# Kernel tuning notes

Hardware: AMD Instinct MI355X
Metric: run time of the kernel (lower is better)

The kernel has to match this reference:

```python
import jax, jax.numpy as jnp
import numpy as np
import math

B, S, D, H = 4, 2048, 1024, 16
HD = D // H  # 64
MOD_DIMS = [("text", 768, 2048), ("image", 1024, 1024), ("audio", 512, 1500), ("video", 2048, 512)]
M = len(MOD_DIMS)
WIN, DEPTH = 3, 8


def _cantor_routes():
    coords = []
    for i in range(M):
        x = i / max(1, M - 1)
        x = max(1e-06, min(x, 1.0 - 1e-06))
        val, f = 0.0, 0.5
        for _ in range(DEPTH):
            x *= 3.0
            d = int(x)
            x -= d
            if d == 2:
                val += f
            f *= 0.5
        coords.append(val)
    c = np.asarray(coords, dtype=np.float32)
    dist = np.abs(c[:, None] - c[None, :])
    # topk smallest distances (stable tie-break like torch ascending sort)
    return np.argsort(dist, axis=1, kind="stable")[:, :WIN]

ROUTES = jnp.asarray(_cantor_routes())


def setup_inputs() -> dict:
    key = jax.random.key(0)
    ks = iter(jax.random.split(key, 32))
    inp = {}
    for name, dim, sl in MOD_DIMS:
        inp[name] = jax.random.normal(next(ks), (B, sl, dim), dtype=jnp.float32)
        inp[f"W_{name}"] = jax.random.normal(next(ks), (D, dim), dtype=jnp.float32) / math.sqrt(dim)
        inp[f"b_{name}"] = jnp.zeros((D,), dtype=jnp.float32)
    inp["mod_emb"] = jax.random.normal(next(ks), (M, D), dtype=jnp.float32) * 0.02
    for nm in ("q", "k", "v", "o"):
        inp[f"W{nm}"] = jax.random.normal(next(ks), (D, D), dtype=jnp.float32) / math.sqrt(D)
        inp[f"b{nm}"] = jnp.zeros((D,), dtype=jnp.float32)
    inp["temperature"] = jnp.asarray(0.07, dtype=jnp.float32)
    return inp


def reference(text, image, audio, video, W_text, b_text, W_image, b_image,
              W_audio, b_audio, W_video, b_video, mod_emb, Wq, bq, Wk, bk,
              Wv, bv, Wo, bo, temperature):
    xs = [text, image, audio, video]
    Ws = [W_text, W_image, W_audio, W_video]
    bs = [b_text, b_image, b_audio, b_video]
    projected = []
    for i in range(M):
        p = xs[i] @ Ws[i].T + bs[i] + mod_emb[i]          # [B, s_i, D]
        p = jnp.pad(p, ((0, 0), (0, S - p.shape[1]), (0, 0)))
        projected.append(p)
    stacked = jnp.stack(projected, axis=1)                # [B, M, S, D]

    def heads(x, W, b):
        return (x @ W.T + b).reshape(B, M, S, H, HD).transpose(0, 3, 1, 2, 4)  # [B,H,M,S,HD]

    Q = heads(stacked, Wq, bq)
    K = heads(stacked, Wk, bk)
    V = heads(stacked, Wv, bv)

    Kn = K[:, :, ROUTES]
    Vn = V[:, :, ROUTES]
    scores = jnp.einsum('bhmsd,bhmwsd->bhmsw', Q, Kn) / (math.sqrt(HD) * jnp.abs(temperature))
    attn = jax.nn.softmax(scores, axis=-1)                # dropout is identity at eval
    out = jnp.einsum('bhmsw,bhmwsd->bhmsd', attn, Vn)     # [B,H,M,S,HD]
    fused = out.mean(axis=2)                              # [B,H,S,HD]
    fused = fused.transpose(0, 2, 1, 3).reshape(B, S, D)
    return fused @ Wo.T + bo
```

## Files before the change

kernel.cpp:

```cpp
#include <hip/hip_runtime.h>

typedef unsigned short u16;
typedef __bf16 bf16x8 __attribute__((ext_vector_type(8)));
typedef u16   u16x8  __attribute__((ext_vector_type(8)));
typedef u16   u16x4  __attribute__((ext_vector_type(4)));
typedef float f32x4  __attribute__((ext_vector_type(4)));

#define RPB 5084
#define SL0 2048
#define SL1 1024
#define SL2 1500
#define SL3 512

__device__ __forceinline__ u16 f2bf(float f) {
  union { float f; unsigned u; } x; x.f = f;
  unsigned u = x.u;
  u += 0x7fffu + ((u >> 16) & 1u);
  return (u16)(u >> 16);
}
__device__ __forceinline__ float bf2f(u16 h) {
  union { unsigned u; float f; } x; x.u = ((unsigned)h) << 16;
  return x.f;
}
__device__ __forceinline__ void gll16(const u16* g, u16* l) {
  __builtin_amdgcn_global_load_lds(
      (const __attribute__((address_space(1))) void*)g,
      (__attribute__((address_space(3))) void*)l, 16, 0, 0);
}


#define NSEG 12
struct CvtSegs {
  const float* src[NSEG];
  u16*         dst[NSEG];
  int          blk_end[NSEG];
  int          blk_base[NSEG];
};
__global__ __launch_bounds__(256) void cvt_multi(CvtSegs segs) {
  int blk = blockIdx.x, seg = 0;
#pragma unroll
  for (int s = 0; s < NSEG; ++s) if (blk >= segs.blk_end[s]) seg = s + 1;
  const float* src = segs.src[seg];
  u16* dst = segs.dst[seg];
  int i = (blk - segs.blk_base[seg]) * 1024 + threadIdx.x * 4;
  f32x4 v = *(const f32x4*)(src + i);
  u16x4 o;
  o[0] = f2bf(v[0]); o[1] = f2bf(v[1]); o[2] = f2bf(v[2]); o[3] = f2bf(v[3]);
  *(u16x4*)(dst + i) = o;
}

template<int STORE_F32>
__global__ __launch_bounds__(256) void gemm_lds(
    const u16* __restrict__ A,
    const u16* __restrict__ B0, const u16* __restrict__ B1, const u16* __restrict__ B2,
    const float* __restrict__ c0, const float* __restrict__ c1, const float* __restrict__ c2,
    void* __restrict__ Cout, int Mr, int K, int ldc)
{
  __shared__ u16 lA0[128 * 32], lA1[128 * 32];
  __shared__ u16 lB0[128 * 32], lB1[128 * 32];
  const int tid  = threadIdx.x;
  const int lane = tid & 63;
  const int wave = tid >> 6;
  const int wr   = (wave >> 1) * 64;
  const int wc   = (wave & 1) * 64;
  const int row0 = blockIdx.y * 128;

  const int wsel = blockIdx.x >> 3;
  const int colL = (blockIdx.x & 7) * 128;
  const u16*   Bw   = (wsel == 0) ? B0 : (wsel == 1) ? B1 : B2;
  const float* bias = (wsel == 0) ? c0 : (wsel == 1) ? c1 : c2;

  const int srow = lane >> 2;
  const int soct = (((lane & 3) ^ ((lane >> 3) & 3))) << 3;
  int ra0 = row0 + wave * 32 + srow;      if (ra0 >= Mr) ra0 = Mr - 1;
  int ra1 = row0 + wave * 32 + srow + 16; if (ra1 >= Mr) ra1 = Mr - 1;
  const u16* pA0 = A + (size_t)ra0 * K + soct;
  const u16* pA1 = A + (size_t)ra1 * K + soct;
  const u16* pB0 = Bw + (size_t)(colL + wave * 32 + srow) * K + soct;
  const u16* pB1 = pB0 + (size_t)16 * K;
  u16* dA0a = &lA0[(wave * 32) * 32];      u16* dA1a = &lA0[(wave * 32 + 16) * 32];
  u16* dA0b = &lA1[(wave * 32) * 32];      u16* dA1b = &lA1[(wave * 32 + 16) * 32];
  u16* dB0a = &lB0[(wave * 32) * 32];      u16* dB1a = &lB0[(wave * 32 + 16) * 32];
  u16* dB0b = &lB1[(wave * 32) * 32];      u16* dB1b = &lB1[(wave * 32 + 16) * 32];

  f32x4 acc[4][4];
#pragma unroll
  for (int i = 0; i < 4; ++i)
#pragma unroll
    for (int j = 0; j < 4; ++j) acc[i][j] = f32x4{0.f, 0.f, 0.f, 0.f};

  const int fr  = lane & 15;
  const int fo  = lane >> 4;
  const int lrd = fr * 32 + (((fo ^ ((fr >> 1) & 3))) << 3);
  const int ca  = (wr >> 4) * 512;
  const int cbb = (wc >> 4) * 512;

  for (int k0 = 0; k0 < K; k0 += 64) {
    __syncthreads();
    gll16(pA0 + k0, dA0a);       gll16(pA1 + k0, dA1a);
    gll16(pB0 + k0, dB0a);       gll16(pB1 + k0, dB1a);
    gll16(pA0 + k0 + 32, dA0b);  gll16(pA1 + k0 + 32, dA1b);
    gll16(pB0 + k0 + 32, dB0b);  gll16(pB1 + k0 + 32, dB1b);
    __syncthreads();

    bf16x8 af[4], bfr[4];
#pragma unroll
    for (int j = 0; j < 4; ++j)
      bfr[j] = *(const bf16x8*)&lB0[cbb + j * 512 + lrd];
#pragma unroll
    for (int i = 0; i < 4; ++i)
      af[i] = *(const bf16x8*)&lA0[ca + i * 512 + lrd];
#pragma unroll
    for (int i = 0; i < 4; ++i)
#pragma unroll
      for (int j = 0; j < 4; ++j)
        acc[i][j] = __builtin_amdgcn_mfma_f32_16x16x32_bf16(af[i], bfr[j], acc[i][j], 0, 0, 0);
#pragma unroll
    for (int j = 0; j < 4; ++j)
      bfr[j] = *(const bf16x8*)&lB1[cbb + j * 512 + lrd];
#pragma unroll
    for (int i = 0; i < 4; ++i)
      af[i] = *(const bf16x8*)&lA1[ca + i * 512 + lrd];
#pragma unroll
    for (int i = 0; i < 4; ++i)
#pragma unroll
      for (int j = 0; j < 4; ++j)
        acc[i][j] = __builtin_amdgcn_mfma_f32_16x16x32_bf16(af[i], bfr[j], acc[i][j], 0, 0, 0);
  }

  const int fc = lane & 15;
  const int rq = (lane >> 4) * 4;
#pragma unroll
  for (int i = 0; i < 4; ++i) {
#pragma unroll
    for (int j = 0; j < 4; ++j) {
      const int cl = wc + j * 16 + fc;
      const float badd = bias[colL + cl];
      const int gc = blockIdx.x * 128 + cl;
#pragma unroll
      for (int reg = 0; reg < 4; ++reg) {
        int gr = row0 + wr + i * 16 + rq + reg;
        if (gr < Mr) {
          float v = acc[i][j][reg] + badd;
          if (STORE_F32) ((float*)Cout)[(size_t)gr * ldc + gc] = v;
          else           ((u16*)Cout)[(size_t)gr * ldc + gc] = f2bf(v);
        }
      }
    }
  }
}

__global__ __launch_bounds__(512, 2) void gemm_qkv_256(
    const u16* __restrict__ A,
    const u16* __restrict__ B0, const u16* __restrict__ B1, const u16* __restrict__ B2,
    const float* __restrict__ c0, const float* __restrict__ c1, const float* __restrict__ c2,
    u16* __restrict__ C, int Mr, int K)
{
  __shared__ u16 lds[4][2][8192];
  const int tid  = threadIdx.x;
  const int lane = tid & 63;
  const int wave = tid >> 6;
  const int wm   = wave >> 2;
  const int wn   = wave & 3;
  const int row0 = blockIdx.y * 256;
  const int cb   = blockIdx.x;
  const int wsel = cb >> 2;
  const int colL = (cb & 3) * 256;
  const u16*   Bw   = (wsel == 0) ? B0 : (wsel == 1) ? B1 : B2;
  const float* bias = (wsel == 0) ? c0 : (wsel == 1) ? c1 : c2;

  const int srow = lane >> 2;
  const int soct = (((lane & 3) ^ ((lane >> 3) & 3))) << 3;
  int ra0 = row0 + wave * 16 + srow;        if (ra0 >= Mr) ra0 = Mr - 1;
  int ra1 = row0 + 128 + wave * 16 + srow;  if (ra1 >= Mr) ra1 = Mr - 1;
  const u16* pA0 = A + (size_t)ra0 * K + soct;
  const u16* pA1 = A + (size_t)ra1 * K + soct;
  const u16* pB0 = Bw + (size_t)(colL + wave * 16 + srow) * K + soct;
  const u16* pB1 = pB0 + (size_t)128 * K;
  const int NS = K >> 5;

#define QSTAGE(slot, k0) do {                                   \
    gll16(pA0 + (k0), (u16*)&lds[slot][0][wave * 512]);         \
    gll16(pA1 + (k0), (u16*)&lds[slot][0][4096 + wave * 512]);  \
    gll16(pB0 + (k0), (u16*)&lds[slot][1][wave * 512]);         \
    gll16(pB1 + (k0), (u16*)&lds[slot][1][4096 + wave * 512]);  \
  } while (0)

  f32x4 acc[8][4];
#pragma unroll
  for (int m = 0; m < 8; ++m)
#pragma unroll
    for (int n = 0; n < 4; ++n) acc[m][n] = f32x4{0.f, 0.f, 0.f, 0.f};

  QSTAGE(0, 0);
  QSTAGE(1, 32);
  QSTAGE(2, 64);

  const int fr  = lane & 15;
  const int fo  = lane >> 4;
  const int lrd = fr * 32 + (((fo ^ ((fr >> 1) & 3))) << 3);
  const int cam = wm * 8 * 512;
  const int cbn = wn * 4 * 512;

#pragma unroll 4
  for (int s = 0; s < NS; ++s) {
    asm volatile("s_waitcnt vmcnt(8)" ::: "memory");
    __builtin_amdgcn_s_barrier();
    asm volatile("" ::: "memory");

    const u16* Ab = &lds[s & 3][0][0];
    const u16* Bb = &lds[s & 3][1][0];
    bf16x8 af[8], bf[4];
#pragma unroll
    for (int n = 0; n < 4; ++n)
      bf[n] = *(const bf16x8*)&Bb[cbn + n * 512 + lrd];
#pragma unroll
    for (int m = 0; m < 8; ++m)
      af[m] = *(const bf16x8*)&Ab[cam + m * 512 + lrd];

    const int s3 = s + 3;
    const int k3 = (s3 < NS ? s3 : NS - 1) << 5;
    QSTAGE(s3 & 3, k3);

#pragma unroll
    for (int m = 0; m < 8; ++m)
#pragma unroll
      for (int n = 0; n < 4; ++n)
        acc[m][n] = __builtin_amdgcn_mfma_f32_16x16x32_bf16(af[m], bf[n], acc[m][n], 0, 0, 0);
  }
#undef QSTAGE

  asm volatile("s_waitcnt vmcnt(0)" ::: "memory");

  const int fc = lane & 15;
  const int rq = (lane >> 4) * 4;
#pragma unroll
  for (int m = 0; m < 8; ++m) {
#pragma unroll
    for (int n = 0; n < 4; ++n) {
      const int cl = wn * 64 + n * 16 + fc;
      const float badd = bias[colL + cl];
      const int gc = cb * 256 + cl;
#pragma unroll
      for (int reg = 0; reg < 4; ++reg) {
        int gr = row0 + wm * 128 + m * 16 + rq + reg;
        if (gr < Mr)
          C[(size_t)gr * 3072 + gc] = f2bf(acc[m][n][reg] + badd);
      }
    }
  }
}

struct ProjSegs {
  const u16*   A[4];
  const u16*   Bw[4];
  const float* b0[4];
  const float* b1[4];
  int Mr[4], K[4], sl[4], obase[4];
  int blk_end[4];
};
__global__ __launch_bounds__(256) void gemm_proj_all(ProjSegs ps, u16* __restrict__ Cout) {
  int blk = blockIdx.x, seg = 0;
#pragma unroll
  for (int s = 0; s < 3; ++s) if (blk >= ps.blk_end[s]) seg = s + 1;
  const int base  = seg ? ps.blk_end[seg - 1] : 0;
  const int local = blk - base;
  const int row0  = (local >> 3) * 128;
  const int col0  = (local & 7) * 128;
  const int Mr = ps.Mr[seg], K = ps.K[seg], sl = ps.sl[seg], obase = ps.obase[seg];
  const u16* A  = ps.A[seg];
  const u16* Bw = ps.Bw[seg];
  const float* bias0 = ps.b0[seg];
  const float* bias1 = ps.b1[seg];

  __shared__ u16 lA0[128 * 32], lA1[128 * 32];
  __shared__ u16 lB0[128 * 32], lB1[128 * 32];
  const int tid  = threadIdx.x;
  const int lane = tid & 63;
  const int wave = tid >> 6;
  const int wr   = (wave >> 1) * 64;
  const int wc   = (wave & 1) * 64;

  const int srow = lane >> 2;
  const int soct = (((lane & 3) ^ ((lane >> 3) & 3))) << 3;
  int ra0 = row0 + wave * 32 + srow;      if (ra0 >= Mr) ra0 = Mr - 1;
  int ra1 = row0 + wave * 32 + srow + 16; if (ra1 >= Mr) ra1 = Mr - 1;
  const u16* pA0 = A + (size_t)ra0 * K + soct;
  const u16* pA1 = A + (size_t)ra1 * K + soct;
  const u16* pB0 = Bw + (size_t)(col0 + wave * 32 + srow) * K + soct;
  const u16* pB1 = pB0 + (size_t)16 * K;
  u16* dA0a = &lA0[(wave * 32) * 32];      u16* dA1a = &lA0[(wave * 32 + 16) * 32];
  u16* dA0b = &lA1[(wave * 32) * 32];      u16* dA1b = &lA1[(wave * 32 + 16) * 32];
  u16* dB0a = &lB0[(wave * 32) * 32];      u16* dB1a = &lB0[(wave * 32 + 16) * 32];
  u16* dB0b = &lB1[(wave * 32) * 32];      u16* dB1b = &lB1[(wave * 32 + 16) * 32];

  f32x4 acc[4][4];
#pragma unroll
  for (int i = 0; i < 4; ++i)
#pragma unroll
    for (int j = 0; j < 4; ++j) acc[i][j] = f32x4{0.f, 0.f, 0.f, 0.f};

  const int fr  = lane & 15;
  const int fo  = lane >> 4;
  const int lrd = fr * 32 + (((fo ^ ((fr >> 1) & 3))) << 3);
  const int ca  = (wr >> 4) * 512;
  const int cbb = (wc >> 4) * 512;

  for (int k0 = 0; k0 < K; k0 += 64) {
    __syncthreads();
    gll16(pA0 + k0, dA0a);       gll16(pA1 + k0, dA1a);
    gll16(pB0 + k0, dB0a);       gll16(pB1 + k0, dB1a);
    gll16(pA0 + k0 + 32, dA0b);  gll16(pA1 + k0 + 32, dA1b);
    gll16(pB0 + k0 + 32, dB0b);  gll16(pB1 + k0 + 32, dB1b);
    __syncthreads();

    bf16x8 af[4], bfr[4];
#pragma unroll
    for (int j = 0; j < 4; ++j)
      bfr[j] = *(const bf16x8*)&lB0[cbb + j * 512 + lrd];
#pragma unroll
    for (int i = 0; i < 4; ++i)
      af[i] = *(const bf16x8*)&lA0[ca + i * 512 + lrd];
#pragma unroll
    for (int i = 0; i < 4; ++i)
#pragma unroll
      for (int j = 0; j < 4; ++j)
        acc[i][j] = __builtin_amdgcn_mfma_f32_16x16x32_bf16(af[i], bfr[j], acc[i][j], 0, 0, 0);
#pragma unroll
    for (int j = 0; j < 4; ++j)
      bfr[j] = *(const bf16x8*)&lB1[cbb + j * 512 + lrd];
#pragma unroll
    for (int i = 0; i < 4; ++i)
      af[i] = *(const bf16x8*)&lA1[ca + i * 512 + lrd];
#pragma unroll
    for (int i = 0; i < 4; ++i)
#pragma unroll
      for (int j = 0; j < 4; ++j)
        acc[i][j] = __builtin_amdgcn_mfma_f32_16x16x32_bf16(af[i], bfr[j], acc[i][j], 0, 0, 0);
  }

  const int fc = lane & 15;
  const int rq = (lane >> 4) * 4;
#pragma unroll
  for (int i = 0; i < 4; ++i) {
#pragma unroll
    for (int j = 0; j < 4; ++j) {
      const int c = col0 + wc + j * 16 + fc;
      const float badd = bias0[c] + bias1[c];
#pragma unroll
      for (int reg = 0; reg < 4; ++reg) {
        int gr = row0 + wr + i * 16 + rq + reg;
        if (gr < Mr) {
          int bb = gr / sl, ss = gr - bb * sl;
          Cout[(size_t)(bb * RPB + obase + ss) * 1024 + c] = f2bf(acc[i][j][reg] + badd);
        }
      }
    }
  }
}

__global__ __launch_bounds__(256) void attn_fuse(
    const u16* __restrict__ QKV,
    u16* __restrict__ fused,
    const float* __restrict__ bq, const float* __restrict__ bk, const float* __restrict__ bv,
    const float* __restrict__ temp_ptr)
{
  const int ROUTE[4][3] = {{0,1,2},{0,1,2},{2,3,0},{3,2,0}};
  const int SLm[4]  = {SL0, SL1, SL2, SL3};
  const int OFFS[4] = {0, 2048, 3072, 4572};
  const int tid  = threadIdx.x;
  const int lane = tid & 63;
  const int wave = tid >> 6;
  const int bs   = blockIdx.x * 2 + (wave >> 1);
  const int s    = bs & 2047;
  const int b    = bs >> 11;
  const int h    = (wave & 1) * 8 + (lane >> 3);
  const int sub  = lane & 7;
  const int dbase = h * 64 + sub * 8;
  const float scale = 1.0f / (8.0f * fabsf(temp_ptr[0]));

  float qf[4][8], kf[4][8], vf[4][8];
#pragma unroll
  for (int r = 0; r < 4; ++r) {
    if (s < SLm[r]) {
      const u16* base = QKV + ((size_t)(b * RPB + OFFS[r] + s)) * 3072 + dbase;
      u16x8 q8 = *(const u16x8*)(base);
      u16x8 k8 = *(const u16x8*)(base + 1024);
      u16x8 v8 = *(const u16x8*)(base + 2048);
#pragma unroll
      for (int i = 0; i < 8; ++i) {
        qf[r][i] = bf2f(q8[i]); kf[r][i] = bf2f(k8[i]); vf[r][i] = bf2f(v8[i]);
      }
    } else {
#pragma unroll
      for (int i = 0; i < 8; ++i) {
        qf[r][i] = bq[dbase + i]; kf[r][i] = bk[dbase + i]; vf[r][i] = bv[dbase + i];
      }
    }
  }

  float acc[8];
#pragma unroll
  for (int i = 0; i < 8; ++i) acc[i] = 0.f;

#pragma unroll
  for (int m = 0; m < 4; ++m) {
    float sc[3];
#pragma unroll
    for (int w = 0; w < 3; ++w) {
      const int r = ROUTE[m][w];
      float d = 0.f;
#pragma unroll
      for (int i = 0; i < 8; ++i) d += qf[m][i] * kf[r][i];
      d += __shfl_xor(d, 1, 64);
      d += __shfl_xor(d, 2, 64);
      d += __shfl_xor(d, 4, 64);
      sc[w] = d * scale;
    }
    float mx = fmaxf(sc[0], fmaxf(sc[1], sc[2]));
    float e0 = __expf(sc[0] - mx), e1 = __expf(sc[1] - mx), e2 = __expf(sc[2] - mx);
    float inv = 1.0f / (e0 + e1 + e2);
    float ws[3] = {e0 * inv, e1 * inv, e2 * inv};
#pragma unroll
    for (int w = 0; w < 3; ++w) {
      const int r = ROUTE[m][w];
#pragma unroll
      for (int i = 0; i < 8; ++i) acc[i] += ws[w] * vf[r][i];
    }
  }
  u16x8 o;
#pragma unroll
  for (int i = 0; i < 8; ++i) o[i] = f2bf(acc[i] * 0.25f);
  *(u16x8*)(fused + (size_t)bs * 1024 + dbase) = o;
}

extern "C" void kernel_launch(void* const* d_in, const int* in_sizes, int n_in,
                              void* d_out, int out_size, void* d_ws, size_t ws_size,
                              hipStream_t stream) {
  const int B = 4, S = 2048, D = 1024;
  const int SL[4]   = {SL0, SL1, SL2, SL3};
  const int DIM[4]  = {768, 1024, 512, 2048};
  const int OFFS[4] = {0, 2048, 3072, 4572};

  const float* x[4]  = {(const float*)d_in[0], (const float*)d_in[3], (const float*)d_in[6], (const float*)d_in[9]};
  const float* Wm[4] = {(const float*)d_in[1], (const float*)d_in[4], (const float*)d_in[7], (const float*)d_in[10]};
  const float* bm[4] = {(const float*)d_in[2], (const float*)d_in[5], (const float*)d_in[8], (const float*)d_in[11]};
  const float* mod_emb = (const float*)d_in[12];
  const float* Wq = (const float*)d_in[13]; const float* bq = (const float*)d_in[14];
  const float* Wk = (const float*)d_in[15]; const float* bk = (const float*)d_in[16];
  const float* Wv = (const float*)d_in[17]; const float* bv = (const float*)d_in[18];
  const float* Wo = (const float*)d_in[19]; const float* bo = (const float*)d_in[20];
  const float* temp = (const float*)d_in[21];

  const int RROWS = B * RPB;
  const size_t stackedB = ((size_t)RROWS * D * 2 + 255) / 256 * 256;
  const size_t qkvB     = ((size_t)RROWS * 3 * D * 2 + 255) / 256 * 256;
  const size_t wB       = ((size_t)D * D * 2 + 255) / 256 * 256;
  size_t wmB[4];
  for (int m = 0; m < 4; ++m) wmB[m] = ((size_t)D * DIM[m] * 2 + 255) / 256 * 256;
  const size_t need = stackedB + qkvB + 4 * wB + wmB[0] + wmB[1] + wmB[2] + wmB[3];
  if (ws_size < need) return;

  char* p = (char*)d_ws;
  u16* stacked = (u16*)p;  p += stackedB;
  char* qkvbase = p;
  u16* qkv     = (u16*)p;  p += qkvB;
  u16* wqb     = (u16*)p;  p += wB;
  u16* wkb     = (u16*)p;  p += wB;
  u16* wvb     = (u16*)p;  p += wB;
  u16* wob     = (u16*)p;  p += wB;
  u16* wmb[4];
  for (int m = 0; m < 4; ++m) { wmb[m] = (u16*)p; p += wmB[m]; }
  u16* fusedb  = stacked;

  u16* xb[4];
  {
    char* q = qkvbase;
    for (int m = 0; m < 4; ++m) {
      xb[m] = (u16*)q;
      q += ((size_t)B * SL[m] * DIM[m] * 2 + 255) / 256 * 256;
    }
  }

  {
    CvtSegs cs;
    const float* srcs[NSEG] = {x[0], x[1], x[2], x[3], Wm[0], Wm[1], Wm[2], Wm[3], Wq, Wk, Wv, Wo};
    u16* dsts[NSEG] = {xb[0], xb[1], xb[2], xb[3], wmb[0], wmb[1], wmb[2], wmb[3], wqb, wkb, wvb, wob};
    int ns[NSEG];
    for (int m = 0; m < 4; ++m) ns[m] = B * SL[m] * DIM[m];
    for (int m = 0; m < 4; ++m) ns[4 + m] = D * DIM[m];
    for (int i = 0; i < 4; ++i) ns[8 + i] = D * D;
    int base = 0;
    for (int i = 0; i < NSEG; ++i) {
      cs.src[i] = srcs[i]; cs.dst[i] = dsts[i];
      cs.blk_base[i] = base;
      base += (ns[i] + 1023) / 1024;
      cs.blk_end[i] = base;
    }
    cvt_multi<<<base, 256, 0, stream>>>(cs);
  }

  {
    const int ord[4] = {3, 1, 0, 2};
    ProjSegs ps;
    int base = 0;
    for (int i = 0; i < 4; ++i) {
      int m = ord[i];
      int Mr = B * SL[m];
      ps.A[i] = xb[m]; ps.Bw[i] = wmb[m];
      ps.b0[i] = bm[m]; ps.b1[i] = mod_emb + m * D;
      ps.Mr[i] = Mr; ps.K[i] = DIM[m]; ps.sl[i] = SL[m]; ps.obase[i] = OFFS[m];
      base += 8 * ((Mr + 127) / 128);
      ps.blk_end[i] = base;
    }
    gemm_proj_all<<<base, 256, 0, stream>>>(ps, stacked);
  }

  {
    dim3 grid(12, (RROWS + 255) / 256);
    gemm_qkv_256<<<grid, 512, 0, stream>>>(stacked, wqb, wkb, wvb, bq, bk, bv,
                                           qkv, RROWS, D);
  }

  attn_fuse<<<(B * S) / 2, 256, 0, stream>>>(qkv, fusedb, bq, bk, bv, temp);

  {
    dim3 grid(8, (B * S) / 128);
    gemm_lds<1><<<grid, 256, 0, stream>>>(fusedb, wob, wob, wob, bo, bo, bo,
                                          d_out, B * S, D, D);
  }
}
```

Before: 470.4 us.

## Restructure QKV GEMM into 8-phase ping-pong pipeline with XCD-aware block remap

```diff
diff --git a/kernel.cpp b/kernel.cpp
--- a/kernel.cpp
+++ b/kernel.cpp
@@ -150,20 +150,22 @@
   }
 }
 
-__global__ __launch_bounds__(512, 2) void gemm_qkv_256(
+__global__ __launch_bounds__(512, 2) void gemm_qkv_8ph(
     const u16* __restrict__ A,
     const u16* __restrict__ B0, const u16* __restrict__ B1, const u16* __restrict__ B2,
     const float* __restrict__ c0, const float* __restrict__ c1, const float* __restrict__ c2,
     u16* __restrict__ C, int Mr, int K)
 {
-  __shared__ u16 lds[4][2][8192];
+  __shared__ u16 lds[2][2][2][16][512];
   const int tid  = threadIdx.x;
   const int lane = tid & 63;
   const int wave = tid >> 6;
   const int wm   = wave >> 2;
   const int wn   = wave & 3;
-  const int row0 = blockIdx.y * 256;
-  const int cb   = blockIdx.x;
+
+  const int v    = (blockIdx.x & 7) * 120 + (blockIdx.x >> 3);
+  const int cb   = v % 12;
+  const int row0 = (v / 12) * 256;
   const int wsel = cb >> 2;
   const int colL = (cb & 3) * 256;
   const u16*   Bw   = (wsel == 0) ? B0 : (wsel == 1) ? B1 : B2;
@@ -177,58 +179,177 @@
   const u16* pA1 = A + (size_t)ra1 * K + soct;
   const u16* pB0 = Bw + (size_t)(colL + wave * 16 + srow) * K + soct;
   const u16* pB1 = pB0 + (size_t)128 * K;
-  const int NS = K >> 5;
-
-#define QSTAGE(slot, k0) do {                                   \
-    gll16(pA0 + (k0), (u16*)&lds[slot][0][wave * 512]);         \
-    gll16(pA1 + (k0), (u16*)&lds[slot][0][4096 + wave * 512]);  \
-    gll16(pB0 + (k0), (u16*)&lds[slot][1][wave * 512]);         \
-    gll16(pB1 + (k0), (u16*)&lds[slot][1][4096 + wave * 512]);  \
-  } while (0)
-
-  f32x4 acc[8][4];
-#pragma unroll
-  for (int m = 0; m < 8; ++m)
-#pragma unroll
-    for (int n = 0; n < 4; ++n) acc[m][n] = f32x4{0.f, 0.f, 0.f, 0.f};
-
-  QSTAGE(0, 0);
-  QSTAGE(1, 32);
-  QSTAGE(2, 64);
+
+#define STA(S, H, KK, KS) gll16(((H) ? pA1 : pA0) + (KK) + (KS) * 32, \
+                                (u16*)&lds[S][0][KS][(H) * 8 + wave][0])
+#define STB(S, H, KK, KS) gll16(((H) ? pB1 : pB0) + (KK) + (KS) * 32, \
+                                (u16*)&lds[S][1][KS][(H) * 8 + wave][0])
 
   const int fr  = lane & 15;
   const int fo  = lane >> 4;
   const int lrd = fr * 32 + (((fo ^ ((fr >> 1) & 3))) << 3);
-  const int cam = wm * 8 * 512;
-  const int cbn = wn * 4 * 512;
-
-#pragma unroll 4
-  for (int s = 0; s < NS; ++s) {
-    asm volatile("s_waitcnt vmcnt(8)" ::: "memory");
-    __builtin_amdgcn_s_barrier();
-    asm volatile("" ::: "memory");
-
-    const u16* Ab = &lds[s & 3][0][0];
-    const u16* Bb = &lds[s & 3][1][0];
-    bf16x8 af[8], bf[4];
-#pragma unroll
-    for (int n = 0; n < 4; ++n)
-      bf[n] = *(const bf16x8*)&Bb[cbn + n * 512 + lrd];
-#pragma unroll
-    for (int m = 0; m < 8; ++m)
-      af[m] = *(const bf16x8*)&Ab[cam + m * 512 + lrd];
-
-    const int s3 = s + 3;
-    const int k3 = (s3 < NS ? s3 : NS - 1) << 5;
-    QSTAGE(s3 & 3, k3);
-
-#pragma unroll
-    for (int m = 0; m < 8; ++m)
-#pragma unroll
-      for (int n = 0; n < 4; ++n)
-        acc[m][n] = __builtin_amdgcn_mfma_f32_16x16x32_bf16(af[m], bf[n], acc[m][n], 0, 0, 0);
-  }
-#undef QSTAGE
+  const int wm8 = wm * 8;
+  const int wn4 = wn * 4;
+
+#define LDA(S, M, KS) (*(const bf16x8*)&lds[S][0][KS][wm8 + (M)][lrd])
+#define LDB(S, N, KS) (*(const bf16x8*)&lds[S][1][KS][wn4 + (N)][lrd])
+
+  f32x4 acc[8][4];
+#pragma unroll
+  for (int m = 0; m < 8; ++m)
+#pragma unroll
+    for (int n = 0; n < 4; ++n) acc[m][n] = f32x4{0.f, 0.f, 0.f, 0.f};
+
+  STA(0, 0, 0, 0);  STA(0, 0, 0, 1);  STA(0, 1, 0, 0);  STA(0, 1, 0, 1);
+  STB(0, 0, 0, 0);  STB(0, 0, 0, 1);  STB(0, 1, 0, 0);  STB(0, 1, 0, 1);
+  STA(1, 0, 64, 0); STA(1, 0, 64, 1); STA(1, 1, 64, 0); STA(1, 1, 64, 1);
+  STB(1, 0, 64, 0); STB(1, 0, 64, 1); STB(1, 1, 64, 0); STB(1, 1, 64, 1);
+  asm volatile("s_waitcnt vmcnt(0)" ::: "memory");
+  __builtin_amdgcn_s_barrier();
+
+  bf16x8 af[4][2], bf[4][2];
+  const int NIT = K >> 7;
+
+#pragma unroll 1
+  for (int i = 0; i < NIT; ++i) {
+    const int k0  = i * 128;
+    const int kc2 = (k0 + 128 <= K - 64) ? k0 + 128 : K - 64;
+    const int kc3 = (k0 + 192 <= K - 64) ? k0 + 192 : K - 64;
+
+#pragma unroll
+    for (int m = 0; m < 4; ++m) { af[m][0] = LDA(0, m, 0); af[m][1] = LDA(0, m, 1); }
+#pragma unroll
+    for (int n = 0; n < 2; ++n) { bf[n][0] = LDB(0, n, 0); bf[n][1] = LDB(0, n, 1); }
+    if (i) { STA(1, 1, k0 + 64, 0); STA(1, 1, k0 + 64, 1); }
+    asm volatile("s_waitcnt lgkmcnt(8)" ::: "memory");
+    __builtin_amdgcn_s_barrier();
+    asm volatile("s_waitcnt lgkmcnt(0)" ::: "memory");
+    __builtin_amdgcn_s_setprio(1);
+#pragma unroll
+    for (int m = 0; m < 4; ++m)
+#pragma unroll
+      for (int n = 0; n < 2; ++n) {
+        acc[m][n] = __builtin_amdgcn_mfma_f32_16x16x32_bf16(af[m][0], bf[n][0], acc[m][n], 0, 0, 0);
+        acc[m][n] = __builtin_amdgcn_mfma_f32_16x16x32_bf16(af[m][1], bf[n][1], acc[m][n], 0, 0, 0);
+      }
+    __builtin_amdgcn_s_setprio(0);
+    __builtin_amdgcn_s_barrier();
+
+#pragma unroll
+    for (int n = 2; n < 4; ++n) { bf[n][0] = LDB(0, n, 0); bf[n][1] = LDB(0, n, 1); }
+    __builtin_amdgcn_s_barrier();
+    asm volatile("s_waitcnt lgkmcnt(0)" ::: "memory");
+    __builtin_amdgcn_s_setprio(1);
+#pragma unroll
+    for (int m = 0; m < 4; ++m)
+#pragma unroll
+      for (int n = 2; n < 4; ++n) {
+        acc[m][n] = __builtin_amdgcn_mfma_f32_16x16x32_bf16(af[m][0], bf[n][0], acc[m][n], 0, 0, 0);
+        acc[m][n] = __builtin_amdgcn_mfma_f32_16x16x32_bf16(af[m][1], bf[n][1], acc[m][n], 0, 0, 0);
+      }
+    __builtin_amdgcn_s_setprio(0);
+    __builtin_amdgcn_s_barrier();
+
+#pragma unroll
+    for (int m = 0; m < 4; ++m) { af[m][0] = LDA(0, 4 + m, 0); af[m][1] = LDA(0, 4 + m, 1); }
+    STB(0, 0, kc2, 0); STB(0, 0, kc2, 1);
+    __builtin_amdgcn_s_barrier();
+    asm volatile("s_waitcnt lgkmcnt(0)" ::: "memory");
+    __builtin_amdgcn_s_setprio(1);
+#pragma unroll
+    for (int m = 0; m < 4; ++m)
+#pragma unroll
+      for (int n = 0; n < 2; ++n) {
+        acc[4 + m][n] = __builtin_amdgcn_mfma_f32_16x16x32_bf16(af[m][0], bf[n][0], acc[4 + m][n], 0, 0, 0);
+        acc[4 + m][n] = __builtin_amdgcn_mfma_f32_16x16x32_bf16(af[m][1], bf[n][1], acc[4 + m][n], 0, 0, 0);
+      }
+    __builtin_amdgcn_s_setprio(0);
+    __builtin_amdgcn_s_barrier();
+
+    STB(0, 1, kc2, 0); STB(0, 1, kc2, 1);
+    STA(0, 0, kc2, 0); STA(0, 0, kc2, 1);
+    asm volatile("s_waitcnt vmcnt(6)" ::: "memory");
+    __builtin_amdgcn_s_barrier();
+    __builtin_amdgcn_s_setprio(1);
+#pragma unroll
+    for (int m = 0; m < 4; ++m)
+#pragma unroll
+      for (int n = 2; n < 4; ++n) {
+        acc[4 + m][n] = __builtin_amdgcn_mfma_f32_16x16x32_bf16(af[m][0], bf[n][0], acc[4 + m][n], 0, 0, 0);
+        acc[4 + m][n] = __builtin_amdgcn_mfma_f32_16x16x32_bf16(af[m][1], bf[n][1], acc[4 + m][n], 0, 0, 0);
+      }
+    __builtin_amdgcn_s_setprio(0);
+    __builtin_amdgcn_s_barrier();
+
+#pragma unroll
+    for (int m = 0; m < 4; ++m) { af[m][0] = LDA(1, m, 0); af[m][1] = LDA(1, m, 1); }
+#pragma unroll
+    for (int n = 0; n < 2; ++n) { bf[n][0] = LDB(1, n, 0); bf[n][1] = LDB(1, n, 1); }
+    STA(0, 1, kc2, 0); STA(0, 1, kc2, 1);
+    asm volatile("s_waitcnt lgkmcnt(8)" ::: "memory");
+    __builtin_amdgcn_s_barrier();
+    asm volatile("s_waitcnt lgkmcnt(0)" ::: "memory");
+    __builtin_amdgcn_s_setprio(1);
+#pragma unroll
+    for (int m = 0; m < 4; ++m)
+#pragma unroll
+      for (int n = 0; n < 2; ++n) {
+        acc[m][n] = __builtin_amdgcn_mfma_f32_16x16x32_bf16(af[m][0], bf[n][0], acc[m][n], 0, 0, 0);
+        acc[m][n] = __builtin_amdgcn_mfma_f32_16x16x32_bf16(af[m][1], bf[n][1], acc[m][n], 0, 0, 0);
+      }
+    __builtin_amdgcn_s_setprio(0);
+    __builtin_amdgcn_s_barrier();
+
+#pragma unroll
+    for (int n = 2; n < 4; ++n) { bf[n][0] = LDB(1, n, 0); bf[n][1] = LDB(1, n, 1); }
+    __builtin_amdgcn_s_barrier();
+    asm volatile("s_waitcnt lgkmcnt(0)" ::: "memory");
+    __builtin_amdgcn_s_setprio(1);
+#pragma unroll
+    for (int m = 0; m < 4; ++m)
+#pragma unroll
+      for (int n = 2; n < 4; ++n) {
+        acc[m][n] = __builtin_amdgcn_mfma_f32_16x16x32_bf16(af[m][0], bf[n][0], acc[m][n], 0, 0, 0);
+        acc[m][n] = __builtin_amdgcn_mfma_f32_16x16x32_bf16(af[m][1], bf[n][1], acc[m][n], 0, 0, 0);
+      }
+    __builtin_amdgcn_s_setprio(0);
+    __builtin_amdgcn_s_barrier();
+
+#pragma unroll
+    for (int m = 0; m < 4; ++m) { af[m][0] = LDA(1, 4 + m, 0); af[m][1] = LDA(1, 4 + m, 1); }
+    STB(1, 0, kc3, 0); STB(1, 0, kc3, 1);
+    __builtin_amdgcn_s_barrier();
+    asm volatile("s_waitcnt lgkmcnt(0)" ::: "memory");
+    __builtin_amdgcn_s_setprio(1);
+#pragma unroll
+    for (int m = 0; m < 4; ++m)
+#pragma unroll
+      for (int n = 0; n < 2; ++n) {
+        acc[4 + m][n] = __builtin_amdgcn_mfma_f32_16x16x32_bf16(af[m][0], bf[n][0], acc[4 + m][n], 0, 0, 0);
+        acc[4 + m][n] = __builtin_amdgcn_mfma_f32_16x16x32_bf16(af[m][1], bf[n][1], acc[4 + m][n], 0, 0, 0);
+      }
+    __builtin_amdgcn_s_setprio(0);
+    __builtin_amdgcn_s_barrier();
+
+    STB(1, 1, kc3, 0); STB(1, 1, kc3, 1);
+    STA(1, 0, kc3, 0); STA(1, 0, kc3, 1);
+    asm volatile("s_waitcnt vmcnt(6)" ::: "memory");
+    __builtin_amdgcn_s_barrier();
+    __builtin_amdgcn_s_setprio(1);
+#pragma unroll
+    for (int m = 0; m < 4; ++m)
+#pragma unroll
+      for (int n = 2; n < 4; ++n) {
+        acc[4 + m][n] = __builtin_amdgcn_mfma_f32_16x16x32_bf16(af[m][0], bf[n][0], acc[4 + m][n], 0, 0, 0);
+        acc[4 + m][n] = __builtin_amdgcn_mfma_f32_16x16x32_bf16(af[m][1], bf[n][1], acc[4 + m][n], 0, 0, 0);
+      }
+    __builtin_amdgcn_s_setprio(0);
+    __builtin_amdgcn_s_barrier();
+  }
+#undef STA
+#undef STB
+#undef LDA
+#undef LDB
 
   asm volatile("s_waitcnt vmcnt(0)" ::: "memory");
 
@@ -517,9 +638,8 @@
   }
 
   {
-    dim3 grid(12, (RROWS + 255) / 256);
-    gemm_qkv_256<<<grid, 512, 0, stream>>>(stacked, wqb, wkb, wvb, bq, bk, bv,
-                                           qkv, RROWS, D);
+    gemm_qkv_8ph<<<12 * ((RROWS + 255) / 256), 512, 0, stream>>>(
+        stacked, wqb, wkb, wvb, bq, bk, bv, qkv, RROWS, D);
   }
 
   attn_fuse<<<(B * S) / 2, 256, 0, stream>>>(qkv, fusedb, bq, bk, bv, temp);
```

After: 470.4 us. About the same (+0.0%).

## Fold modality projections into QKV weights and drop the stacked intermediate GEMM

Applied to the files above, without the earlier changes.

```diff
diff --git a/kernel.cpp b/kernel.cpp
--- a/kernel.cpp
+++ b/kernel.cpp
@@ -29,7 +29,7 @@
 }
 
 
-#define NSEG 12
+#define NSEG 8
 struct CvtSegs {
   const float* src[NSEG];
   u16*         dst[NSEG];
@@ -47,6 +47,150 @@
   u16x4 o;
   o[0] = f2bf(v[0]); o[1] = f2bf(v[1]); o[2] = f2bf(v[2]); o[3] = f2bf(v[3]);
   *(u16x4*)(dst + i) = o;
+}
+
+struct TrSegs { const float* src[4]; u16* dst[4]; int dimc[4]; int blk_end[4]; };
+__global__ __launch_bounds__(256) void cvt_transpose(TrSegs ts) {
+  __shared__ float t[32][33];
+  int blk = blockIdx.x, seg = 0;
+#pragma unroll
+  for (int s = 0; s < 3; ++s) if (blk >= ts.blk_end[s]) seg = s + 1;
+  int base  = seg ? ts.blk_end[seg - 1] : 0;
+  int local = blk - base;
+  int DIMc  = ts.dimc[seg];
+  int tpr   = DIMc >> 5;
+  int tr = local / tpr, tc = local - tr * tpr;
+  const float* src = ts.src[seg];
+  u16* dst = ts.dst[seg];
+  int r0 = tr * 32, c0 = tc * 32;
+  int cx = threadIdx.x & 31, ry = threadIdx.x >> 5;
+#pragma unroll
+  for (int k = 0; k < 4; ++k)
+    t[ry + 8 * k][cx] = src[(size_t)(r0 + ry + 8 * k) * DIMc + c0 + cx];
+  __syncthreads();
+#pragma unroll
+  for (int k = 0; k < 4; ++k)
+    dst[(size_t)(c0 + ry + 8 * k) * 1024 + r0 + cx] = f2bf(t[cx][ry + 8 * k]);
+}
+
+__global__ __launch_bounds__(256) void bias_prep(
+    const float* __restrict__ Wq, const float* __restrict__ Wk, const float* __restrict__ Wv,
+    const float* __restrict__ bq, const float* __restrict__ bk, const float* __restrict__ bv,
+    const float* __restrict__ bm0, const float* __restrict__ bm1,
+    const float* __restrict__ bm2, const float* __restrict__ bm3,
+    const float* __restrict__ emb, float* __restrict__ out )
+{
+  const int wid  = blockIdx.x * 4 + (threadIdx.x >> 6);
+  const int lane = threadIdx.x & 63;
+  const int m = wid / 3072, n = wid - m * 3072;
+  const float* wr_ = (n < 1024) ? Wq + (size_t)n * 1024
+                   : (n < 2048) ? Wk + (size_t)(n - 1024) * 1024
+                                : Wv + (size_t)(n - 2048) * 1024;
+  const float  br  = (n < 1024) ? bq[n] : (n < 2048) ? bk[n - 1024] : bv[n - 2048];
+  const float* bmp = (m == 0) ? bm0 : (m == 1) ? bm1 : (m == 2) ? bm2 : bm3;
+  const float* ep  = emb + (size_t)m * 1024;
+  const int k0 = lane * 16;
+  float s = 0.f;
+#pragma unroll
+  for (int i = 0; i < 16; ++i) s += wr_[k0 + i] * (bmp[k0 + i] + ep[k0 + i]);
+  s += __shfl_xor(s, 1);  s += __shfl_xor(s, 2);  s += __shfl_xor(s, 4);
+  s += __shfl_xor(s, 8);  s += __shfl_xor(s, 16); s += __shfl_xor(s, 32);
+  if (lane == 0) out[(size_t)m * 3072 + n] = s + br;
+}
+
+struct WpSegs { const u16* Bw[4]; u16* Cout[4]; int Nn[4]; int blk_end[4]; };
+__global__ __launch_bounds__(256) void gemm_wprep(WpSegs wsg, const u16* __restrict__ A) {
+  int blk = blockIdx.x, seg = 0;
+#pragma unroll
+  for (int s = 0; s < 3; ++s) if (blk >= wsg.blk_end[s]) seg = s + 1;
+  const int base  = seg ? wsg.blk_end[seg - 1] : 0;
+  const int local = blk - base;
+  const int Nn  = wsg.Nn[seg];
+  const int ctm = Nn >> 7;
+  const int rt  = local / ctm;
+  const int row0 = rt * 128, col0 = (local - rt * ctm) * 128;
+  const int K = 1024;
+  const u16* Bw = wsg.Bw[seg];
+  u16* Cout = wsg.Cout[seg];
+
+  __shared__ u16 lA0[128 * 32], lA1[128 * 32];
+  __shared__ u16 lB0[128 * 32], lB1[128 * 32];
+  const int tid  = threadIdx.x;
+  const int lane = tid & 63;
+  const int wave = tid >> 6;
+  const int wr   = (wave >> 1) * 64;
+  const int wc   = (wave & 1) * 64;
+
+  const int srow = lane >> 2;
+  const int soct = (((lane & 3) ^ ((lane >> 3) & 3))) << 3;
+  const u16* pA0 = A + (size_t)(row0 + wave * 32 + srow) * K + soct;
+  const u16* pA1 = pA0 + (size_t)16 * K;
+  const u16* pB0 = Bw + (size_t)(col0 + wave * 32 + srow) * K + soct;
+  const u16* pB1 = pB0 + (size_t)16 * K;
+  u16* dA0a = &lA0[(wave * 32) * 32];      u16* dA1a = &lA0[(wave * 32 + 16) * 32];
+  u16* dA0b = &lA1[(wave * 32) * 32];      u16* dA1b = &lA1[(wave * 32 + 16) * 32];
+  u16* dB0a = &lB0[(wave * 32) * 32];      u16* dB1a = &lB0[(wave * 32 + 16) * 32];
+  u16* dB0b = &lB1[(wave * 32) * 32];      u16* dB1b = &lB1[(wave * 32 + 16) * 32];
+
+  f32x4 acc[4][4];
+#pragma unroll
+  for (int i = 0; i < 4; ++i)
+#pragma unroll
+    for (int j = 0; j < 4; ++j) acc[i][j] = f32x4{0.f, 0.f, 0.f, 0.f};
+
+  const int fr  = lane & 15;
+  const int fo  = lane >> 4;
+  const int lrd = fr * 32 + (((fo ^ ((fr >> 1) & 3))) << 3);
+  const int ca  = (wr >> 4) * 512;
+  const int cbb = (wc >> 4) * 512;
+
+  for (int k0 = 0; k0 < K; k0 += 64) {
+    __syncthreads();
+    gll16(pA0 + k0, dA0a);       gll16(pA1 + k0, dA1a);
+    gll16(pB0 + k0, dB0a);       gll16(pB1 + k0, dB1a);
+    gll16(pA0 + k0 + 32, dA0b);  gll16(pA1 + k0 + 32, dA1b);
+    gll16(pB0 + k0 + 32, dB0b);  gll16(pB1 + k0 + 32, dB1b);
+    __syncthreads();
+
+    bf16x8 af[4], bfr[4];
+#pragma unroll
+    for (int j = 0; j < 4; ++j)
+      bfr[j] = *(const bf16x8*)&lB0[cbb + j * 512 + lrd];
+#pragma unroll
+    for (int i = 0; i < 4; ++i)
+      af[i] = *(const bf16x8*)&lA0[ca + i * 512 + lrd];
+#pragma unroll
+    for (int i = 0; i < 4; ++i)
+#pragma unroll
+      for (int j = 0; j < 4; ++j)
+        acc[i][j] = __builtin_amdgcn_mfma_f32_16x16x32_bf16(af[i], bfr[j], acc[i][j], 0, 0, 0);
+#pragma unroll
+    for (int j = 0; j < 4; ++j)
+      bfr[j] = *(const bf16x8*)&lB1[cbb + j * 512 + lrd];
+#pragma unroll
+    for (int i = 0; i < 4; ++i)
+      af[i] = *(const bf16x8*)&lA1[ca + i * 512 + lrd];
+#pragma unroll
+    for (int i = 0; i < 4; ++i)
+#pragma unroll
+      for (int j = 0; j < 4; ++j)
+        acc[i][j] = __builtin_amdgcn_mfma_f32_16x16x32_bf16(af[i], bfr[j], acc[i][j], 0, 0, 0);
+  }
+
+  const int fc = lane & 15;
+  const int rq = (lane >> 4) * 4;
+#pragma unroll
+  for (int i = 0; i < 4; ++i) {
+#pragma unroll
+    for (int j = 0; j < 4; ++j) {
+      const int gc = col0 + wc + j * 16 + fc;
+#pragma unroll
+      for (int reg = 0; reg < 4; ++reg) {
+        int gr = row0 + wr + i * 16 + rq + reg;
+        Cout[(size_t)gr * Nn + gc] = f2bf(acc[i][j][reg]);
+      }
+    }
+  }
 }
 
 template<int STORE_F32>
@@ -150,24 +294,32 @@
   }
 }
 
-__global__ __launch_bounds__(512, 2) void gemm_qkv_256(
-    const u16* __restrict__ A,
-    const u16* __restrict__ B0, const u16* __restrict__ B1, const u16* __restrict__ B2,
-    const float* __restrict__ c0, const float* __restrict__ c1, const float* __restrict__ c2,
-    u16* __restrict__ C, int Mr, int K)
-{
+struct QkvSegs {
+  const u16*   A[4];
+  const u16*   Bw[4];
+  const float* bias[4];
+  int Mr[4], K[4], sl[4], obase[4], blk_end[4];
+};
+__global__ __launch_bounds__(512, 2) void gemm_qkv_seg(QkvSegs qs, u16* __restrict__ C) {
   __shared__ u16 lds[4][2][8192];
+  int blk = blockIdx.x, seg = 0;
+#pragma unroll
+  for (int s = 0; s < 3; ++s) if (blk >= qs.blk_end[s]) seg = s + 1;
+  const int base  = seg ? qs.blk_end[seg - 1] : 0;
+  const int local = blk - base;
+  const int cbt   = local % 12;
+  const int row0  = (local / 12) * 256;
+  const int colL  = cbt * 256;
+  const int Mr = qs.Mr[seg], K = qs.K[seg], sl = qs.sl[seg], obase = qs.obase[seg];
+  const u16* A  = qs.A[seg];
+  const u16* Bw = qs.Bw[seg];
+  const float* bias = qs.bias[seg];
+
   const int tid  = threadIdx.x;
   const int lane = tid & 63;
   const int wave = tid >> 6;
   const int wm   = wave >> 2;
   const int wn   = wave & 3;
-  const int row0 = blockIdx.y * 256;
-  const int cb   = blockIdx.x;
-  const int wsel = cb >> 2;
-  const int colL = (cb & 3) * 256;
-  const u16*   Bw   = (wsel == 0) ? B0 : (wsel == 1) ? B1 : B2;
-  const float* bias = (wsel == 0) ? c0 : (wsel == 1) ? c1 : c2;
 
   const int srow = lane >> 2;
   const int soct = (((lane & 3) ^ ((lane >> 3) & 3))) << 3;
@@ -240,119 +392,13 @@
     for (int n = 0; n < 4; ++n) {
       const int cl = wn * 64 + n * 16 + fc;
       const float badd = bias[colL + cl];
-      const int gc = cb * 256 + cl;
+      const int gc = colL + cl;
 #pragma unroll
       for (int reg = 0; reg < 4; ++reg) {
         int gr = row0 + wm * 128 + m * 16 + rq + reg;
-        if (gr < Mr)
-          C[(size_t)gr * 3072 + gc] = f2bf(acc[m][n][reg] + badd);
-      }
-    }
-  }
-}
-
-struct ProjSegs {
-  const u16*   A[4];
-  const u16*   Bw[4];
-  const float* b0[4];
-  const float* b1[4];
-  int Mr[4], K[4], sl[4], obase[4];
-  int blk_end[4];
-};
-__global__ __launch_bounds__(256) void gemm_proj_all(ProjSegs ps, u16* __restrict__ Cout) {
-  int blk = blockIdx.x, seg = 0;
-#pragma unroll
-  for (int s = 0; s < 3; ++s) if (blk >= ps.blk_end[s]) seg = s + 1;
-  const int base  = seg ? ps.blk_end[seg - 1] : 0;
-  const int local = blk - base;
-  const int row0  = (local >> 3) * 128;
-  const int col0  = (local & 7) * 128;
-  const int Mr = ps.Mr[seg], K = ps.K[seg], sl = ps.sl[seg], obase = ps.obase[seg];
-  const u16* A  = ps.A[seg];
-  const u16* Bw = ps.Bw[seg];
-  const float* bias0 = ps.b0[seg];
-  const float* bias1 = ps.b1[seg];
-
-  __shared__ u16 lA0[128 * 32], lA1[128 * 32];
-  __shared__ u16 lB0[128 * 32], lB1[128 * 32];
-  const int tid  = threadIdx.x;
-  const int lane = tid & 63;
-  const int wave = tid >> 6;
-  const int wr   = (wave >> 1) * 64;
-  const int wc   = (wave & 1) * 64;
-
-  const int srow = lane >> 2;
-  const int soct = (((lane & 3) ^ ((lane >> 3) & 3))) << 3;
-  int ra0 = row0 + wave * 32 + srow;      if (ra0 >= Mr) ra0 = Mr - 1;
-  int ra1 = row0 + wave * 32 + srow + 16; if (ra1 >= Mr) ra1 = Mr - 1;
-  const u16* pA0 = A + (size_t)ra0 * K + soct;
-  const u16* pA1 = A + (size_t)ra1 * K + soct;
-  const u16* pB0 = Bw + (size_t)(col0 + wave * 32 + srow) * K + soct;
-  const u16* pB1 = pB0 + (size_t)16 * K;
-  u16* dA0a = &lA0[(wave * 32) * 32];      u16* dA1a = &lA0[(wave * 32 + 16) * 32];
-  u16* dA0b = &lA1[(wave * 32) * 32];      u16* dA1b = &lA1[(wave * 32 + 16) * 32];
-  u16* dB0a = &lB0[(wave * 32) * 32];      u16* dB1a = &lB0[(wave * 32 + 16) * 32];
-  u16* dB0b = &lB1[(wave * 32) * 32];      u16* dB1b = &lB1[(wave * 32 + 16) * 32];
-
-  f32x4 acc[4][4];
-#pragma unroll
-  for (int i = 0; i < 4; ++i)
-#pragma unroll
-    for (int j = 0; j < 4; ++j) acc[i][j] = f32x4{0.f, 0.f, 0.f, 0.f};
-
-  const int fr  = lane & 15;
-  const int fo  = lane >> 4;
-  const int lrd = fr * 32 + (((fo ^ ((fr >> 1) & 3))) << 3);
-  const int ca  = (wr >> 4) * 512;
-  const int cbb = (wc >> 4) * 512;
-
-  for (int k0 = 0; k0 < K; k0 += 64) {
-    __syncthreads();
-    gll16(pA0 + k0, dA0a);       gll16(pA1 + k0, dA1a);
-    gll16(pB0 + k0, dB0a);       gll16(pB1 + k0, dB1a);
-    gll16(pA0 + k0 + 32, dA0b);  gll16(pA1 + k0 + 32, dA1b);
-    gll16(pB0 + k0 + 32, dB0b);  gll16(pB1 + k0 + 32, dB1b);
-    __syncthreads();
-
-    bf16x8 af[4], bfr[4];
-#pragma unroll
-    for (int j = 0; j < 4; ++j)
-      bfr[j] = *(const bf16x8*)&lB0[cbb + j * 512 + lrd];
-#pragma unroll
-    for (int i = 0; i < 4; ++i)
-      af[i] = *(const bf16x8*)&lA0[ca + i * 512 + lrd];
-#pragma unroll
-    for (int i = 0; i < 4; ++i)
-#pragma unroll
-      for (int j = 0; j < 4; ++j)
-        acc[i][j] = __builtin_amdgcn_mfma_f32_16x16x32_bf16(af[i], bfr[j], acc[i][j], 0, 0, 0);
-#pragma unroll
-    for (int j = 0; j < 4; ++j)
-      bfr[j] = *(const bf16x8*)&lB1[cbb + j * 512 + lrd];
-#pragma unroll
-    for (int i = 0; i < 4; ++i)
-      af[i] = *(const bf16x8*)&lA1[ca + i * 512 + lrd];
-#pragma unroll
-    for (int i = 0; i < 4; ++i)
-#pragma unroll
-      for (int j = 0; j < 4; ++j)
-        acc[i][j] = __builtin_amdgcn_mfma_f32_16x16x32_bf16(af[i], bfr[j], acc[i][j], 0, 0, 0);
-  }
-
-  const int fc = lane & 15;
-  const int rq = (lane >> 4) * 4;
-#pragma unroll
-  for (int i = 0; i < 4; ++i) {
-#pragma unroll
-    for (int j = 0; j < 4; ++j) {
-      const int c = col0 + wc + j * 16 + fc;
-      const float badd = bias0[c] + bias1[c];
-#pragma unroll
-      for (int reg = 0; reg < 4; ++reg) {
-        int gr = row0 + wr + i * 16 + rq + reg;
         if (gr < Mr) {
           int bb = gr / sl, ss = gr - bb * sl;
-          Cout[(size_t)(bb * RPB + obase + ss) * 1024 + c] = f2bf(acc[i][j][reg] + badd);
+          C[(size_t)(bb * RPB + obase + ss) * 3072 + gc] = f2bf(acc[m][n][reg] + badd);
         }
       }
     }
@@ -453,43 +499,42 @@
   const float* temp = (const float*)d_in[21];
 
   const int RROWS = B * RPB;
-  const size_t stackedB = ((size_t)RROWS * D * 2 + 255) / 256 * 256;
-  const size_t qkvB     = ((size_t)RROWS * 3 * D * 2 + 255) / 256 * 256;
-  const size_t wB       = ((size_t)D * D * 2 + 255) / 256 * 256;
-  size_t wmB[4];
-  for (int m = 0; m < 4; ++m) wmB[m] = ((size_t)D * DIM[m] * 2 + 255) / 256 * 256;
-  const size_t need = stackedB + qkvB + 4 * wB + wmB[0] + wmB[1] + wmB[2] + wmB[3];
+  const size_t qkvB   = ((size_t)RROWS * 3 * D * 2 + 255) / 256 * 256;
+  size_t xbB[4], wmTB[4], wqkvmB[4];
+  size_t xbTot = 0, wmTTot = 0, wqkvmTot = 0;
+  for (int m = 0; m < 4; ++m) {
+    xbB[m]    = ((size_t)B * SL[m] * DIM[m] * 2 + 255) / 256 * 256;  xbTot    += xbB[m];
+    wmTB[m]   = ((size_t)DIM[m] * D * 2 + 255) / 256 * 256;          wmTTot   += wmTB[m];
+    wqkvmB[m] = ((size_t)3 * D * DIM[m] * 2 + 255) / 256 * 256;      wqkvmTot += wqkvmB[m];
+  }
+  const size_t wB   = (size_t)D * D * 2;
+  const size_t bqmB = ((size_t)4 * 3 * D * 4 + 255) / 256 * 256;
+  const size_t need = qkvB + xbTot + wmTTot + 3 * wB + wB + wqkvmTot + bqmB;
   if (ws_size < need) return;
 
   char* p = (char*)d_ws;
-  u16* stacked = (u16*)p;  p += stackedB;
-  char* qkvbase = p;
-  u16* qkv     = (u16*)p;  p += qkvB;
-  u16* wqb     = (u16*)p;  p += wB;
-  u16* wkb     = (u16*)p;  p += wB;
-  u16* wvb     = (u16*)p;  p += wB;
-  u16* wob     = (u16*)p;  p += wB;
-  u16* wmb[4];
-  for (int m = 0; m < 4; ++m) { wmb[m] = (u16*)p; p += wmB[m]; }
-  u16* fusedb  = stacked;
-
+  u16* qkv = (u16*)p;  p += qkvB;
   u16* xb[4];
-  {
-    char* q = qkvbase;
-    for (int m = 0; m < 4; ++m) {
-      xb[m] = (u16*)q;
-      q += ((size_t)B * SL[m] * DIM[m] * 2 + 255) / 256 * 256;
-    }
-  }
+  char* xbBase = p;
+  for (int m = 0; m < 4; ++m) { xb[m] = (u16*)p; p += xbB[m]; }
+  u16* wmT[4];
+  for (int m = 0; m < 4; ++m) { wmT[m] = (u16*)p; p += wmTB[m]; }
+  u16* wqb = (u16*)p;  p += wB;
+  u16* wkb = (u16*)p;  p += wB;
+  u16* wvb = (u16*)p;  p += wB;
+  u16* wob = (u16*)p;  p += wB;
+  u16* wqkvm[4];
+  for (int m = 0; m < 4; ++m) { wqkvm[m] = (u16*)p; p += wqkvmB[m]; }
+  float* bqm = (float*)p;  p += bqmB;
+  u16* fusedb = (u16*)xbBase;
 
   {
     CvtSegs cs;
-    const float* srcs[NSEG] = {x[0], x[1], x[2], x[3], Wm[0], Wm[1], Wm[2], Wm[3], Wq, Wk, Wv, Wo};
-    u16* dsts[NSEG] = {xb[0], xb[1], xb[2], xb[3], wmb[0], wmb[1], wmb[2], wmb[3], wqb, wkb, wvb, wob};
+    const float* srcs[NSEG] = {x[0], x[1], x[2], x[3], Wq, Wk, Wv, Wo};
+    u16* dsts[NSEG] = {xb[0], xb[1], xb[2], xb[3], wqb, wkb, wvb, wob};
     int ns[NSEG];
     for (int m = 0; m < 4; ++m) ns[m] = B * SL[m] * DIM[m];
-    for (int m = 0; m < 4; ++m) ns[4 + m] = D * DIM[m];
-    for (int i = 0; i < 4; ++i) ns[8 + i] = D * D;
+    for (int i = 0; i < 4; ++i) ns[4 + i] = D * D;
     int base = 0;
     for (int i = 0; i < NSEG; ++i) {
       cs.src[i] = srcs[i]; cs.dst[i] = dsts[i];
@@ -501,25 +546,45 @@
   }
 
   {
+    TrSegs ts;
+    int base = 0;
+    for (int m = 0; m < 4; ++m) {
+      ts.src[m] = Wm[m]; ts.dst[m] = wmT[m]; ts.dimc[m] = DIM[m];
+      base += (D / 32) * (DIM[m] / 32);
+      ts.blk_end[m] = base;
+    }
+    cvt_transpose<<<base, 256, 0, stream>>>(ts);
+  }
+
+  bias_prep<<<3072, 256, 0, stream>>>(Wq, Wk, Wv, bq, bk, bv,
+                                      bm[0], bm[1], bm[2], bm[3], mod_emb, bqm);
+
+  {
     const int ord[4] = {3, 1, 0, 2};
-    ProjSegs ps;
+    WpSegs wsg;
+    int base = 0;
+    for (int i = 0; i < 4; ++i) {
+      int m = ord[i];
+      wsg.Bw[i] = wmT[m]; wsg.Cout[i] = wqkvm[m]; wsg.Nn[i] = DIM[m];
+      base += (3 * D / 128) * (DIM[m] / 128);
+      wsg.blk_end[i] = base;
+    }
+    gemm_wprep<<<base, 256, 0, stream>>>(wsg, wqb);
+  }
+
+  {
+    const int ord[4] = {3, 1, 0, 2};
+    QkvSegs qsg;
     int base = 0;
     for (int i = 0; i < 4; ++i) {
       int m = ord[i];
       int Mr = B * SL[m];
-      ps.A[i] = xb[m]; ps.Bw[i] = wmb[m];
-      ps.b0[i] = bm[m]; ps.b1[i] = mod_emb + m * D;
-      ps.Mr[i] = Mr; ps.K[i] = DIM[m]; ps.sl[i] = SL[m]; ps.obase[i] = OFFS[m];
-      base += 8 * ((Mr + 127) / 128);
-      ps.blk_end[i] = base;
-    }
-    gemm_proj_all<<<base, 256, 0, stream>>>(ps, stacked);
-  }
-
-  {
-    dim3 grid(12, (RROWS + 255) / 256);
-    gemm_qkv_256<<<grid, 512, 0, stream>>>(stacked, wqb, wkb, wvb, bq, bk, bv,
-                                           qkv, RROWS, D);
+      qsg.A[i] = xb[m]; qsg.Bw[i] = wqkvm[m]; qsg.bias[i] = bqm + m * 3072;
+      qsg.Mr[i] = Mr; qsg.K[i] = DIM[m]; qsg.sl[i] = SL[m]; qsg.obase[i] = OFFS[m];
+      base += 12 * ((Mr + 255) / 256);
+      qsg.blk_end[i] = base;
+    }
+    gemm_qkv_seg<<<base, 512, 0, stream>>>(qsg, qkv);
   }
 
   attn_fuse<<<(B * S) / 2, 256, 0, stream>>>(qkv, fusedb, bq, bk, bv, temp);
```

Result: no change. 469.7 us (-0.1%).
